# Kernel tuning notes

Measured on AMD Instinct MI355X. Metric: run time of the kernel, lower is better.

## Reference

```python
import jax, jax.numpy as jnp
import numpy as np

SCALE = 2
K = 5          # up_kernel
GROUPS = 1     # up_group
COMP = 64      # compressed_channels


def _conv2d(x, w, b, padding):
    out = jax.lax.conv_general_dilated(
        x, w, window_strides=(1, 1),
        padding=[(padding, padding), (padding, padding)],
        dimension_numbers=('NCHW', 'OIHW', 'NCHW'))
    return out + b[None, :, None, None]


def _pixel_shuffle(x, r):
    b, crr, h, w = x.shape
    c = crr // (r * r)
    x = x.reshape(b, c, r, r, h, w)
    x = x.transpose(0, 1, 4, 2, 5, 3)  # b, c, h, r, w, r
    return x.reshape(b, c, h * r, w * r)


def setup_inputs() -> dict:
    key = jax.random.key(0)
    k1, k2, k3 = jax.random.split(key, 3)
    C = 256
    x = jax.random.normal(k1, (4, C, 128, 128), dtype=jnp.float32)
    mask_ch = SCALE * SCALE * K * K * GROUPS  # 100
    W1 = jax.random.normal(k2, (COMP, C, 1, 1), dtype=jnp.float32) * 0.05
    b1 = jnp.zeros((COMP,), dtype=jnp.float32)
    W2 = jax.random.normal(k3, (mask_ch, COMP, 3, 3), dtype=jnp.float32) * 0.05
    b2 = jnp.zeros((mask_ch,), dtype=jnp.float32)
    return {'x': x, 'W1': W1, 'b1': b1, 'W2': W2, 'b2': b2}


def reference(x, W1, b1, W2, b2):
    b, c, h, w = x.shape
    s, k, g = SCALE, K, GROUPS
    H, W = h * s, w * s
    # channel compressor (1x1) + mask encoder (3x3, pad 1)
    feat = _conv2d(x, W1, b1, 0)
    mask = _conv2d(feat, W2, b2, 1)            # (b, s^2*k^2*g, h, w)
    mask = _pixel_shuffle(mask, s)             # (b, k^2*g, H, W)
    mask = mask.reshape(b, g, k * k, H, W)
    mask = jax.nn.softmax(mask, axis=2)
    # nearest upsample
    x_up = jnp.repeat(jnp.repeat(x, s, axis=2), s, axis=3)  # (b, c, H, W)
    pad = k // 2
    xp = jnp.pad(x_up, ((0, 0), (0, 0), (pad, pad), (pad, pad)))
    xg = xp.reshape(b, g, c // g, H + 2 * pad, W + 2 * pad)
    # fused gather-multiply-reduce over the k*k window (avoids the huge unfold tensor)
    out = jnp.zeros((b, g, c // g, H, W), x.dtype)
    for i in range(k):
        for j in range(k):
            out = out + xg[:, :, :, i:i + H, j:j + W] * mask[:, :, None, i * k + j]
    return out.reshape(b, c, H, W)
```

## Files before the change

### kernel.cpp

```cpp
#include <hip/hip_runtime.h>

#define HW 16384
#define CIN 256
#define NCOMP 64
#define MASKC 100
#define NB 4
#define COPAD 112
#define KSTEPS 18

typedef __attribute__((ext_vector_type(8))) short bf16x8;
typedef __attribute__((ext_vector_type(4))) float f32x4;

__device__ inline ushort f2bf(float f) {
  uint x = __float_as_uint(f);
  return (ushort)((x + 0x7fffu + ((x >> 16) & 1u)) >> 16);
}

__global__ __launch_bounds__(256) void conv1x1_mfma(const float* __restrict__ x,
    const ushort* __restrict__ W1b, const float* __restrict__ b1,
    ushort* __restrict__ feat_t) {
  int tid = threadIdx.x, bid = blockIdx.x;
  int b = bid >> 7, h = bid & 127;
  int wave = tid >> 6, lane = tid & 63;
  int l15 = lane & 15, l4 = lane >> 4;

  const float* xb = x + ((size_t)b << 22) + h * 128;

  f32x4 acc[2][4];
  #pragma unroll
  for (int u = 0; u < 2; u++)
    #pragma unroll
    for (int mt = 0; mt < 4; mt++) acc[u][mt] = (f32x4){0.f, 0.f, 0.f, 0.f};

  #pragma unroll
  for (int s = 0; s < 8; s++) {
    int k0 = s * 32 + l4 * 8;
    bf16x8 af[4];
    #pragma unroll
    for (int mt = 0; mt < 4; mt++)
      af[mt] = *(const bf16x8*)(W1b + (((mt * 8 + s) << 6) + lane) * 8);
    #pragma unroll
    for (int u = 0; u < 2; u++) {
      int n = wave * 32 + u * 16 + l15;
      union { bf16x8 v; ushort us[8]; } bf;
      #pragma unroll
      for (int j = 0; j < 8; j++)
        bf.us[j] = f2bf(xb[((size_t)(k0 + j) << 14) + n]);
      #pragma unroll
      for (int mt = 0; mt < 4; mt++)
        acc[u][mt] = __builtin_amdgcn_mfma_f32_16x16x32_bf16(af[mt], bf.v, acc[u][mt], 0, 0, 0);
    }
  }

  ushort* fbase = feat_t + (((size_t)(b << 14) + h * 128) << 6);
  #pragma unroll
  for (int u = 0; u < 2; u++) {
    int n = wave * 32 + u * 16 + l15;
    ushort* fb = fbase + ((size_t)n << 6);
    #pragma unroll
    for (int mt = 0; mt < 4; mt++) {
      float4 bv = *(const float4*)(b1 + mt * 16 + l4 * 4);
      const float* bvp = (const float*)&bv;
      uint u0 = (uint)f2bf(acc[u][mt][0] + bvp[0]) | ((uint)f2bf(acc[u][mt][1] + bvp[1]) << 16);
      uint u1 = (uint)f2bf(acc[u][mt][2] + bvp[2]) | ((uint)f2bf(acc[u][mt][3] + bvp[3]) << 16);
      uint2 st; st.x = u0; st.y = u1;
      *(uint2*)(fb + mt * 16 + l4 * 4) = st;
    }
  }
}

__global__ __launch_bounds__(256) void wprep_k(const float* __restrict__ W2,
    const float* __restrict__ W1, ushort* __restrict__ Wr,
    ushort* __restrict__ W1b) {
  int i = blockIdx.x * 256 + threadIdx.x;
  if (i < 64512) {
    int e = i & 7, lane = (i >> 3) & 63, sm = i >> 9;
    int s = sm % 18, mt = sm / 18;
    int l15 = lane & 15, l4 = lane >> 4;
    int co = mt * 16 + l15;
    int ci = (s & 1) * 32 + l4 * 8 + e;
    int k = s >> 1;
    float v = (co < MASKC) ? W2[(co * 64 + ci) * 9 + k] : 0.f;
    Wr[i] = f2bf(v);
  } else if (i < 64512 + 16384) {
    int j = i - 64512;
    int e = j & 7, lane = (j >> 3) & 63, sm = j >> 9;
    int s = sm & 7, mt = sm >> 3;
    int l15 = lane & 15, l4 = lane >> 4;
    int co = mt * 16 + l15;
    int ci = s * 32 + l4 * 8 + e;
    W1b[j] = f2bf(W1[co * 256 + ci]);
  }
}

__global__ __launch_bounds__(512) void conv3x3_combine(const ushort* __restrict__ feat_t,
    const ushort* __restrict__ Wr, const float* __restrict__ b2,
    const float* __restrict__ x, float* __restrict__ out) {
  __shared__ __align__(16) char smem[100 * 129 * 4];
  __shared__ float b2s[COPAD];
  int tid = threadIdx.x;
  int wid = (blockIdx.x & 7) * 64 + (blockIdx.x >> 3);
  int b = wid >> 7, h = wid & 127;
  int wave = tid >> 6, lane = tid & 63;
  int l15 = lane & 15, l4 = lane >> 4;

  if (tid < COPAD) b2s[tid] = (tid < MASKC) ? b2[tid] : 0.f;

  f32x4 acc[7];
  #pragma unroll
  for (int mt = 0; mt < 7; mt++) acc[mt] = (f32x4){0.f, 0.f, 0.f, 0.f};

  int cb = wave * 16;
  const ushort* fb = feat_t + (((size_t)b << 14) << 6);

  #pragma unroll
  for (int s = 0; s < KSTEPS; s++) {
    const int k = s >> 1;
    const int r = k / 3;
    const int dx = k % 3 - 1;
    const int ci0 = (s & 1) * 32;

    int hh = h - 1 + r;
    int gc = cb + l15 + dx;
    bf16x8 bfrag = {0, 0, 0, 0, 0, 0, 0, 0};
    if ((unsigned)hh < 128u && (unsigned)gc < 128u)
      bfrag = *(const bf16x8*)(fb + (((size_t)(hh * 128 + gc)) << 6) + ci0 + l4 * 8);

    #pragma unroll
    for (int mt = 0; mt < 7; mt++) {
      bf16x8 afrag = *(const bf16x8*)(Wr + (((mt * 18 + s) << 6) + lane) * 8);
      acc[mt] = __builtin_amdgcn_mfma_f32_16x16x32_bf16(afrag, bfrag, acc[mt], 0, 0, 0);
    }
  }

  float* ldsM = (float*)smem;
  #pragma unroll
  for (int mt = 0; mt < 7; mt++)
    #pragma unroll
    for (int q = 0; q < 4; q++) {
      int co = mt * 16 + l4 * 4 + q;
      if (co < MASKC)
        ldsM[co * 129 + cb + l15] = acc[mt][q] + b2s[co];
    }
  __syncthreads();

  float wr9[9];
  int px = tid & 127, rr = tid >> 7;
  {
    #pragma unroll
    for (int i = 0; i < 9; i++) wr9[i] = 0.f;

    float m[25], mx = -1e30f;
    #pragma unroll
    for (int kk = 0; kk < 25; kk++) {
      m[kk] = ldsM[(kk * 4 + rr) * 129 + px];
      mx = fmaxf(mx, m[kk]);
    }
    float s = 0.f;
    #pragma unroll
    for (int kk = 0; kk < 25; kk++) { m[kk] = __expf(m[kk] - mx); s += m[kk]; }
    float inv = 1.f / s;
    const int r1 = rr >> 1, r2 = rr & 1;
    #pragma unroll
    for (int i = 0; i < 5; i++)
      #pragma unroll
      for (int j = 0; j < 5; j++) {
        const int dy = (r1 + i - 2) >> 1;
        const int dxx = (r2 + j - 2) >> 1;
        wr9[(dy + 1) * 3 + (dxx + 1)] += m[i * 5 + j] * inv;
      }

    #pragma unroll
    for (int dy = -1; dy <= 1; dy++) {
      bool vy = (unsigned)(h + dy) < 128u;
      #pragma unroll
      for (int dxx = -1; dxx <= 1; dxx++) {
        bool vx = (unsigned)(px + dxx) < 128u;
        if (!(vy && vx)) wr9[(dy + 1) * 3 + dxx + 1] = 0.f;
      }
    }
  }
  __syncthreads();

  float* wlds = (float*)smem;
  {
    #pragma unroll
    for (int i = 0; i < 9; i++) wlds[px * 37 + rr * 9 + i] = wr9[i];
  }
  __syncthreads();

  {
    int p = tid & 127, quarter = tid >> 7;
    float wc[36];
    #pragma unroll
    for (int i = 0; i < 36; i++) wc[i] = wlds[p * 37 + i];

    int ys[3] = {max(h - 1, 0) * 128, h * 128, min(h + 1, 127) * 128};
    int xs[3] = {max(p - 1, 0), p, min(p + 1, 127)};
    const float* xbase = x + ((size_t)b << 22);
    float* ob = out + (((size_t)b * CIN) << 16) + ((2 * h) << 8) + 2 * p;

    #pragma unroll 4
    for (int cc = 0; cc < 64; cc++) {
      int c = cc * 4 + quarter;
      const float* xc = xbase + ((size_t)c << 14);
      float v[9];
      #pragma unroll
      for (int yy = 0; yy < 3; yy++)
        #pragma unroll
        for (int xx = 0; xx < 3; xx++)
          v[yy * 3 + xx] = xc[ys[yy] + xs[xx]];
      float a0 = 0.f, a1 = 0.f, a2 = 0.f, a3 = 0.f;
      #pragma unroll
      for (int k = 0; k < 9; k++) {
        a0 += wc[0 * 9 + k] * v[k];
        a1 += wc[1 * 9 + k] * v[k];
        a2 += wc[2 * 9 + k] * v[k];
        a3 += wc[3 * 9 + k] * v[k];
      }
      float* oc = ob + ((size_t)c << 16);
      float2 e0; e0.x = a0; e0.y = a1;
      float2 e1; e1.x = a2; e1.y = a3;
      *(float2*)(oc) = e0;
      *(float2*)(oc + 256) = e1;
    }
  }
}

extern "C" void kernel_launch(void* const* d_in, const int* in_sizes, int n_in,
                              void* d_out, int out_size, void* d_ws, size_t ws_size,
                              hipStream_t stream) {
  const float* x  = (const float*)d_in[0];
  const float* W1 = (const float*)d_in[1];
  const float* b1 = (const float*)d_in[2];
  const float* W2 = (const float*)d_in[3];
  const float* b2 = (const float*)d_in[4];
  float* out  = (float*)d_out;

  char* ws = (char*)d_ws;
  ushort* feat_t = (ushort*)ws;
  ushort* Wr     = (ushort*)(ws + 8388608);
  ushort* W1b    = (ushort*)(ws + 8388608 + 129024);

  wprep_k<<<316, 256, 0, stream>>>(W2, W1, Wr, W1b);
  conv1x1_mfma<<<NB * 128, 256, 0, stream>>>(x, W1b, b1, feat_t);
  conv3x3_combine<<<NB * 128, 512, 0, stream>>>(feat_t, Wr, b2, x, out);
}
```

Measured before the change: 112.6 us.

## Process two adjacent pixels per thread with shared 4-wide x loads and packed FMA

Restructures the final combine loop so each thread handles two neighbouring source pixels, sharing one unaligned 4-float load per row and remapping the 9-tap weights into a 4-tap window with edge shifts. Accumulation uses 2-wide float vectors so the compiler can emit packed FMAs, and the output stores widen from float2 to float4. Launch bounds now request 4 blocks per CU. The aim is fewer global loads and instructions per output. The cost is a larger weight register footprint (96 floats), which may pressure occupancy or cause spills.

```diff
diff --git a/kernel.cpp b/kernel.cpp
--- a/kernel.cpp
+++ b/kernel.cpp
@@ -10,6 +10,8 @@
 
 typedef __attribute__((ext_vector_type(8))) short bf16x8;
 typedef __attribute__((ext_vector_type(4))) float f32x4;
+typedef __attribute__((ext_vector_type(2))) float f32x2;
+typedef __attribute__((ext_vector_type(4), aligned(4))) float f4u;
 
 __device__ inline ushort f2bf(float f) {
   uint x = __float_as_uint(f);
@@ -93,7 +95,7 @@
   }
 }
 
-__global__ __launch_bounds__(512) void conv3x3_combine(const ushort* __restrict__ feat_t,
+__global__ __launch_bounds__(512, 4) void conv3x3_combine(const ushort* __restrict__ feat_t,
     const ushort* __restrict__ Wr, const float* __restrict__ b2,
     const float* __restrict__ x, float* __restrict__ out) {
   __shared__ __align__(16) char smem[100 * 129 * 4];
@@ -190,39 +192,64 @@
   __syncthreads();
 
   {
-    int p = tid & 127, quarter = tid >> 7;
-    float wc[36];
-    #pragma unroll
-    for (int i = 0; i < 36; i++) wc[i] = wlds[p * 37 + i];
+    int pp = tid & 63, g = tid >> 6;
+    int w0 = pp * 2;
+    int sh = (w0 == 0) ? -1 : ((w0 == 126) ? 1 : 0);
+    int cc0 = w0 - 1 - sh;
+
+    float a36[36], b36[36];
+    #pragma unroll
+    for (int i = 0; i < 36; i++) a36[i] = wlds[w0 * 37 + i];
+    #pragma unroll
+    for (int i = 0; i < 36; i++) b36[i] = wlds[(w0 + 1) * 37 + i];
+
+    bool s0 = (sh == 0), smi = (sh == -1);
+    f32x2 wp[4][3][4];
+    #pragma unroll
+    for (int r = 0; r < 4; r++)
+      #pragma unroll
+      for (int dy = 0; dy < 3; dy++)
+        #pragma unroll
+        for (int i = 0; i < 4; i++) {
+          float v0 = (i <= 2) ? a36[r * 9 + dy * 3 + i] : 0.f;
+          float vm = (i + 1 <= 2) ? a36[r * 9 + dy * 3 + i + 1] : 0.f;
+          float vp = (i >= 1) ? a36[r * 9 + dy * 3 + i - 1] : 0.f;
+          float wA = s0 ? v0 : (smi ? vm : vp);
+          float u0 = (i >= 1) ? b36[r * 9 + dy * 3 + i - 1] : 0.f;
+          float um = (i <= 2) ? b36[r * 9 + dy * 3 + i] : 0.f;
+          float up = (i >= 2) ? b36[r * 9 + dy * 3 + i - 2] : 0.f;
+          float wB = s0 ? u0 : (smi ? um : up);
+          f32x2 w2; w2.x = wA; w2.y = wB;
+          wp[r][dy][i] = w2;
+        }
 
     int ys[3] = {max(h - 1, 0) * 128, h * 128, min(h + 1, 127) * 128};
-    int xs[3] = {max(p - 1, 0), p, min(p + 1, 127)};
-    const float* xbase = x + ((size_t)b << 22);
-    float* ob = out + (((size_t)b * CIN) << 16) + ((2 * h) << 8) + 2 * p;
-
-    #pragma unroll 4
-    for (int cc = 0; cc < 64; cc++) {
-      int c = cc * 4 + quarter;
+    const float* xbase = x + ((size_t)b << 22) + cc0;
+    float* ob = out + (((size_t)b * CIN) << 16) + ((2 * h) << 8) + 2 * w0;
+
+    #pragma unroll 2
+    for (int cc = 0; cc < 32; cc++) {
+      int c = cc * 8 + g;
       const float* xc = xbase + ((size_t)c << 14);
-      float v[9];
-      #pragma unroll
-      for (int yy = 0; yy < 3; yy++)
+      f32x2 acc2[4];
+      #pragma unroll
+      for (int r = 0; r < 4; r++) acc2[r] = (f32x2){0.f, 0.f};
+      #pragma unroll
+      for (int dy = 0; dy < 3; dy++) {
+        f4u f = *(const f4u*)(xc + ys[dy]);
         #pragma unroll
-        for (int xx = 0; xx < 3; xx++)
-          v[yy * 3 + xx] = xc[ys[yy] + xs[xx]];
-      float a0 = 0.f, a1 = 0.f, a2 = 0.f, a3 = 0.f;
-      #pragma unroll
-      for (int k = 0; k < 9; k++) {
-        a0 += wc[0 * 9 + k] * v[k];
-        a1 += wc[1 * 9 + k] * v[k];
-        a2 += wc[2 * 9 + k] * v[k];
-        a3 += wc[3 * 9 + k] * v[k];
+        for (int i = 0; i < 4; i++) {
+          f32x2 fv; fv.x = f[i]; fv.y = f[i];
+          #pragma unroll
+          for (int r = 0; r < 4; r++)
+            acc2[r] += wp[r][dy][i] * fv;
+        }
       }
       float* oc = ob + ((size_t)c << 16);
-      float2 e0; e0.x = a0; e0.y = a1;
-      float2 e1; e1.x = a2; e1.y = a3;
-      *(float2*)(oc) = e0;
-      *(float2*)(oc + 256) = e1;
+      float4 o0; o0.x = acc2[0].x; o0.y = acc2[1].x; o0.z = acc2[0].y; o0.w = acc2[1].y;
+      float4 o1; o1.x = acc2[2].x; o1.y = acc2[3].x; o1.z = acc2[2].y; o1.w = acc2[3].y;
+      *(float4*)(oc) = o0;
+      *(float4*)(oc + 256) = o1;
     }
   }
 }
```

After: 127.8 us. +13.5%, slower.
